# Performance work log

Measured on AMD Instinct MI355X. Metric: run time of the kernel, lower is better.

Reference implementation:

```python
import jax, jax.numpy as jnp
import numpy as np

P = 16        # patch size
SIM = 0.3     # similarity threshold (forward default arg `sim`)
STY_STD = 1000.0


def patchify(imgs):
    # (N,3,H,W) -> (N, h*w, p*p*3)
    N, C, H, W = imgs.shape
    h, w = H // P, W // P
    x = imgs.reshape(N, C, h, P, w, P)
    x = jnp.einsum('nchpwq->nhwpqc', x)
    return x.reshape(N, h * w, P * P * C)


def setup_inputs() -> dict:
    key = jax.random.key(0)
    k1, k2, k3, k4 = jax.random.split(key, 4)
    N, L, D = 2, 196, 768
    x = jax.random.normal(k1, (N, L + 1, D), dtype=jnp.float32)
    imgs = jax.random.normal(k2, (N, 3, 224, 224), dtype=jnp.float32)
    # torch trunc_normal_(std=1000, a=-2, b=2) == truncated normal on [-2,2]
    learnable_sty = (jax.random.truncated_normal(
        k3, -2.0 / STY_STD, 2.0 / STY_STD, (N, L, L, 1), dtype=jnp.float32) * STY_STD)
    noise = jax.random.normal(k4, (N, L, L, 1), dtype=jnp.float32)
    return {"x": x, "imgs": imgs, "learnable_sty": learnable_sty, "noise": noise}


def reference(x, imgs, learnable_sty, noise):
    imgs = patchify(imgs)                                   # (N, L, 768)
    cls_tokens, x = x[:, :1], x[:, 1:]
    N, L, D = x.shape

    # per-patch normalization (torch.var default is unbiased -> ddof=1)
    mean = imgs.mean(axis=-1, keepdims=True)
    var = jnp.var(imgs, axis=-1, keepdims=True, ddof=1)
    imgs_n = (imgs - mean) / jnp.sqrt(var + 1e-6)
    nrm = jnp.linalg.norm(imgs_n, axis=-1)                  # (N, L)
    Sim = jnp.einsum('aik,ajk->aij', imgs_n, imgs_n) / (nrm[:, :, None] * nrm[:, None, :])

    M0 = jnp.triu((Sim > SIM).astype(jnp.float32))          # (N, L, L), binary
    rows = jnp.arange(L)

    def body(i, M):
        # original loop breaks when sum == N*L; we freeze M once that holds
        done = M.sum() == N * L
        mask = (M[:, i, :] == 0).astype(M.dtype)            # (N, L)
        # rows <= i unchanged (M*M == M for binary), rows > i masked
        upd = jnp.where(rows[None, :, None] > i, M * mask[:, None, :], M)
        return jnp.where(done, M, upd)

    M = jax.lax.fori_loop(0, L - 1, body, M0)

    # decompose: phase (con) keeps grad, amplitude (sty) is detached
    fft = jnp.fft.fftn(x, axes=(-1,))
    con, sty = jnp.angle(fft), jnp.abs(fft)
    sty_d = jax.lax.stop_gradient(sty)

    avg_sum = (M[..., None] * sty_d[:, None, :, :]).sum(axis=2)   # (N, L, D)
    sty_mask = (avg_sum > 0).astype(jnp.float32)                   # (N, L, D)
    num = M.sum(axis=2)[..., None]                                 # (N, L, 1)
    avg = avg_sum / jnp.clip(num, 1e-7, None)                      # (N, L, D)
    std = jnp.sqrt(
        (M[..., None] * (sty_d[:, None, :, :] - avg[:, :, None, :]) ** 2).sum(axis=2)
        / jnp.clip(num, 1e-7, None))                               # (N, L, D)

    sty_para = sty_mask[:, None, :, :] * learnable_sty             # (N, L, L, D)
    sty_para = sty_para / jnp.clip(sty_para.sum(axis=2, keepdims=True), 1e-7, None)
    various = noise * std[:, None, :, :] + avg[:, None, :, :]      # (N, L, L, D)
    sum_sty = (sty_para * various).sum(axis=2)                     # (N, L, D)

    # compose: ifft(amp * e^{i phase}), torch .float() keeps the real part
    out = jnp.real(jnp.fft.ifftn(sum_sty * jnp.exp(1j * con), axes=(-1,))).astype(jnp.float32)
    return jnp.concatenate((cls_tokens, out), axis=1)
```

## Files before the change

kernel.cpp:

```cpp
#include <hip/hip_runtime.h>
#include <math.h>

typedef unsigned long long u64;

#define NBATCH 2
#define LTOK 196
#define DDIM 768
#define NROWS (NBATCH*LTOK)
#define NLD (NBATCH*LTOK*DDIM)

#define PI_F 3.14159265358979323846f
#define S3 0.86602540378443864676f

#define RTILE 14
#define JCH 4
#define JLEN 49
#define NCOMB (NBATCH*14*3*JCH)
#define GRIDB NROWS
#define NGRP 7
#define GSZ 56

#define SGRP 8
#define NSIMG 25
#define NSIMB (NBATCH*NSIMG)

__device__ __forceinline__ float aldf(const float* p) {
  unsigned u = __hip_atomic_load((const unsigned*)p, __ATOMIC_RELAXED,
                                 __HIP_MEMORY_SCOPE_AGENT);
  return __uint_as_float(u);
}
__device__ __forceinline__ void astf(float* p, float v) {
  __hip_atomic_store((unsigned*)p, __float_as_uint(v), __ATOMIC_RELAXED,
                     __HIP_MEMORY_SCOPE_AGENT);
}
__device__ __forceinline__ u64 ald64(const u64* p) {
  return __hip_atomic_load(p, __ATOMIC_RELAXED, __HIP_MEMORY_SCOPE_AGENT);
}
__device__ __forceinline__ void ast64(u64* p, u64 v) {
  __hip_atomic_store(p, v, __ATOMIC_RELAXED, __HIP_MEMORY_SCOPE_AGENT);
}

union ShMem {
  struct { float re[768]; float im[768]; float2 tw[128]; } fft;
  struct { double rs[4]; double rq[4]; float mu; float sc; } pat;
  struct { float simT[768][SGRP]; u64 gmask[SGRP][4]; int last; } sim2;
  struct { u64 Ml[NROWS*4]; int red[4]; int done; } gr;
  struct { u64 mrow[4]; } st;
  struct { float lsr[RTILE][JLEN], lnr[RTILE][JLEN]; } cmb;
};

__device__ __forceinline__ void gbar(unsigned* bar, int slot) {
  __syncthreads();
  if (threadIdx.x == 0) {
    unsigned* root = bar + (size_t)(slot * 8) * 32;
    unsigned* grp  = bar + (size_t)(slot * 8 + 1 + (blockIdx.x / GSZ)) * 32;
    if (__hip_atomic_fetch_add(grp, 1u, __ATOMIC_RELAXED,
                               __HIP_MEMORY_SCOPE_AGENT) == GSZ - 1u) {
      __hip_atomic_fetch_add(root, 1u, __ATOMIC_RELAXED,
                             __HIP_MEMORY_SCOPE_AGENT);
    }
    while (__hip_atomic_load(root, __ATOMIC_RELAXED,
                             __HIP_MEMORY_SCOPE_AGENT) < (unsigned)NGRP) {
      __builtin_amdgcn_s_sleep(8);
    }
  }
  __syncthreads();
}

__device__ __forceinline__ void fft_butterfly(float* re, float* im,
                                              const float2* T,
                                              int tau, int s, int half) {
  int sub = tau >> 7;
  int b = tau & 127;
  int j = b & (half - 1);
  int p0 = (sub << 8) + ((b >> (s - 1)) << s) + j;
  int p1 = p0 + half;
  float2 w = T[j << (8 - s)];
  float xr = re[p1], xi = im[p1];
  float tr = w.x * xr - w.y * xi;
  float ti = w.x * xi + w.y * xr;
  float ur = re[p0], ui = im[p0];
  re[p0] = ur + tr; im[p0] = ui + ti;
  re[p1] = ur - tr; im[p1] = ui - ti;
}

__device__ __forceinline__ void fft_stages(float* re, float* im,
                                           const float2* T, int t) {
#pragma unroll
  for (int s = 1; s <= 8; s++) {
    int half = 1 << (s - 1);
    fft_butterfly(re, im, T, t, s, half);
    if (t < 128) fft_butterfly(re, im, T, t + 256, s, half);
    __syncthreads();
  }
}

__device__ void greedy_block(u64* __restrict__ Mb, ShMem& sh) {
  int t = threadIdx.x;
  for (int w = t; w < NROWS * 4; w += 256) sh.gr.Ml[w] = ald64(&Mb[w]);
  __syncthreads();
  for (int i = 0; i < LTOK - 1; i++) {
    int s = 0;
    for (int w = t; w < NROWS * 4; w += 256) s += __popcll(sh.gr.Ml[w]);
#pragma unroll
    for (int o = 32; o > 0; o >>= 1) s += __shfl_down(s, o);
    if ((t & 63) == 0) sh.gr.red[t >> 6] = s;
    __syncthreads();
    if (t == 0)
      sh.gr.done = ((sh.gr.red[0] + sh.gr.red[1] + sh.gr.red[2] + sh.gr.red[3]) == NROWS) ? 1 : 0;
    __syncthreads();
    if (sh.gr.done) break;
    for (int w = t; w < NROWS * 4; w += 256) {
      int a = w / (LTOK * 4);
      int rem = w - a * (LTOK * 4);
      int r = rem >> 2, wi = rem & 3;
      if (r > i) sh.gr.Ml[w] &= ~sh.gr.Ml[(a * LTOK + i) * 4 + wi];
    }
    __syncthreads();
  }
  for (int w = t; w < NROWS * 4; w += 256) ast64(&Mb[w], sh.gr.Ml[w]);
}

__global__ __launch_bounds__(256, 2) void mega(
    const float* __restrict__ imgs, const float* __restrict__ x,
    const float* __restrict__ ls, const float* __restrict__ nz,
    float* __restrict__ out,
    float* __restrict__ uT, float* __restrict__ sty,
    float* __restrict__ phre, float* __restrict__ phim,
    float* __restrict__ sstd, float* __restrict__ smsk,
    float* __restrict__ numP, float* __restrict__ denP,
    u64* __restrict__ Mb, unsigned* __restrict__ bar) {
  __shared__ ShMem sh;
  const int t = threadIdx.x;
  const int blk = blockIdx.x;
  const int a = blk / LTOK, i = blk - (blk / LTOK) * LTOK;
  unsigned* ctr = bar + 32 * 32;

  {
    int hh = i / 14, ww = i - hh * 14;
    float loc[3];
    double s = 0.0, sq = 0.0;
#pragma unroll
    for (int e = 0; e < 3; e++) {
      int d = t + (e << 8);
      int p = d / 48, r = d - p * 48;
      int q2 = r / 3, c = r - q2 * 3;
      float val = imgs[((size_t)(a * 3 + c) * 224 + (hh * 16 + p)) * 224 + (ww * 16 + q2)];
      loc[e] = val;
      s += (double)val;
      sq += (double)val * (double)val;
    }
#pragma unroll
    for (int o = 32; o > 0; o >>= 1) { s += __shfl_down(s, o); sq += __shfl_down(sq, o); }
    if ((t & 63) == 0) { sh.pat.rs[t >> 6] = s; sh.pat.rq[t >> 6] = sq; }
    __syncthreads();
    if (t == 0) {
      double S = sh.pat.rs[0] + sh.pat.rs[1] + sh.pat.rs[2] + sh.pat.rs[3];
      double Q = sh.pat.rq[0] + sh.pat.rq[1] + sh.pat.rq[2] + sh.pat.rq[3];
      double mean = S / 768.0;
      double ss = Q - S * S / 768.0;
      if (ss < 1e-30) ss = 1e-30;
      sh.pat.mu = (float)mean;
      sh.pat.sc = (float)(1.0 / sqrt(ss));
    }
    __syncthreads();
    float mu = sh.pat.mu, sc = sh.pat.sc;
    int col = a * LTOK + i;
#pragma unroll
    for (int e = 0; e < 3; e++) {
      int d = t + (e << 8);
      astf(&uT[(size_t)d * NROWS + col], (loc[e] - mu) * sc);
    }
  }
  __syncthreads();

  {
    if (t < 128) {
      float sn, cs;
      __sincosf(-2.0f * PI_F * (float)t / 256.0f, &sn, &cs);
      sh.fft.tw[t] = make_float2(cs, sn);
    }
    size_t row = ((size_t)a * (LTOK + 1) + 1 + i) * DDIM;
#pragma unroll
    for (int e = 0; e < 3; e++) {
      int d = t + (e << 8);
      int m = d / 3, r = d - 3 * m;
      int p = (r << 8) + (__brev((unsigned)m) >> 24);
      sh.fft.re[p] = x[row + d];
      sh.fft.im[p] = 0.f;
    }
    __syncthreads();
    fft_stages(sh.fft.re, sh.fft.im, sh.fft.tw, t);
    float a0r = sh.fft.re[t],       a0i = sh.fft.im[t];
    float a1r = sh.fft.re[256 + t], a1i = sh.fft.im[256 + t];
    float a2r = sh.fft.re[512 + t], a2i = sh.fft.im[512 + t];
    float sn, cs;
    __sincosf(-2.0f * PI_F * (float)t / 768.0f, &sn, &cs);
    float2 w1 = make_float2(cs, sn);
    float2 w2 = make_float2(cs * cs - sn * sn, 2.f * cs * sn);
    float b1r = a1r * w1.x - a1i * w1.y, b1i = a1r * w1.y + a1i * w1.x;
    float b2r = a2r * w2.x - a2i * w2.y, b2i = a2r * w2.y + a2i * w2.x;
    float Xr[3], Xi[3];
    Xr[0] = a0r + b1r + b2r;
    Xi[0] = a0i + b1i + b2i;
    Xr[1] = a0r + (-0.5f * b1r + S3 * b1i) + (-0.5f * b2r - S3 * b2i);
    Xi[1] = a0i + (-0.5f * b1i - S3 * b1r) + (-0.5f * b2i + S3 * b2r);
    Xr[2] = a0r + (-0.5f * b1r - S3 * b1i) + (-0.5f * b2r + S3 * b2i);
    Xi[2] = a0i + (-0.5f * b1i + S3 * b1r) + (-0.5f * b2i - S3 * b2r);
    size_t ob = ((size_t)a * LTOK + i) * DDIM + t;
#pragma unroll
    for (int s2 = 0; s2 < 3; s2++) {
      float mag = sqrtf(Xr[s2] * Xr[s2] + Xi[s2] * Xi[s2]);
      size_t o = ob + (s2 << 8);
      astf(&sty[o], mag);
      if (mag > 0.f) { astf(&phre[o], Xr[s2] / mag); astf(&phim[o], Xi[s2] / mag); }
      else           { astf(&phre[o], 1.f);          astf(&phim[o], 0.f);          }
    }
  }
  gbar(bar, 0);

  if (blk < NSIMB) {
    int sa = blk / NSIMG, grp = blk - sa * NSIMG;
    int i0 = grp * SGRP;
    int nrow = (LTOK - i0 < SGRP) ? (LTOK - i0) : SGRP;
    int base = sa * LTOK + i0;
    for (int idx = t; idx < SGRP * 4; idx += 256) ((u64*)sh.sim2.gmask)[idx] = 0ull;
    for (int idx = t; idx < 768 * SGRP; idx += 256) {
      int d = idx >> 3, r = idx & 7;
      sh.sim2.simT[d][r] = (r < nrow) ? aldf(&uT[(size_t)d * NROWS + base + r]) : 0.f;
    }
    __syncthreads();
    int j = i0 + t;
    if (j < LTOK) {
      const float* colp = uT + sa * LTOK + j;
      float acc[SGRP];
#pragma unroll
      for (int k = 0; k < SGRP; k++) acc[k] = 0.f;
      for (int d0 = 0; d0 < 768; d0 += 16) {
        float cv[16];
#pragma unroll
        for (int q = 0; q < 16; q++) cv[q] = aldf(colp + (size_t)(d0 + q) * NROWS);
#pragma unroll
        for (int q = 0; q < 16; q++) {
          float4 A0 = *(const float4*)&sh.sim2.simT[d0 + q][0];
          float4 A1 = *(const float4*)&sh.sim2.simT[d0 + q][4];
          acc[0] += A0.x * cv[q]; acc[1] += A0.y * cv[q];
          acc[2] += A0.z * cv[q]; acc[3] += A0.w * cv[q];
          acc[4] += A1.x * cv[q]; acc[5] += A1.y * cv[q];
          acc[6] += A1.z * cv[q]; acc[7] += A1.w * cv[q];
        }
      }
#pragma unroll
      for (int k = 0; k < SGRP; k++) {
        int ii = i0 + k;
        if (k < nrow && j >= ii && acc[k] > 0.3f)
          atomicOr(&sh.sim2.gmask[k][j >> 6], 1ull << (j & 63));
      }
    }
    __syncthreads();
    if (t < nrow * 4)
      ast64(&Mb[((size_t)(base + (t >> 2))) * 4 + (t & 3)], sh.sim2.gmask[t >> 2][t & 3]);
    __syncthreads();
    if (t == 0)
      sh.sim2.last = (__hip_atomic_fetch_add(ctr, 1u, __ATOMIC_RELAXED,
                                             __HIP_MEMORY_SCOPE_AGENT) == NSIMB - 1u) ? 1 : 0;
    __syncthreads();
    int amlast = sh.sim2.last;
    __syncthreads();
    if (amlast) greedy_block(Mb, sh);
  }
  gbar(bar, 1);

  {
    float* savg = uT;
    if (t < 4) sh.st.mrow[t] = ald64(&Mb[((size_t)a * LTOK + i) * 4 + t]);
    __syncthreads();
    int num = __popcll(sh.st.mrow[0]) + __popcll(sh.st.mrow[1]) +
              __popcll(sh.st.mrow[2]) + __popcll(sh.st.mrow[3]);
    float fnum = fmaxf((float)num, 1e-7f);
    float acc0 = 0.f, acc1 = 0.f, acc2 = 0.f;
    for (int w = 0; w < 4; w++) {
      u64 m = sh.st.mrow[w];
      while (m) {
        int b = __ffsll(m) - 1; m &= (m - 1);
        int jj = (w << 6) + b;
        const float* sr = sty + ((size_t)a * LTOK + jj) * DDIM;
        acc0 += aldf(&sr[t]); acc1 += aldf(&sr[t + 256]); acc2 += aldf(&sr[t + 512]);
      }
    }
    float av0 = acc0 / fnum, av1 = acc1 / fnum, av2 = acc2 / fnum;
    float sq0 = 0.f, sq1 = 0.f, sq2 = 0.f;
    for (int w = 0; w < 4; w++) {
      u64 m = sh.st.mrow[w];
      while (m) {
        int b = __ffsll(m) - 1; m &= (m - 1);
        int jj = (w << 6) + b;
        const float* sr = sty + ((size_t)a * LTOK + jj) * DDIM;
        float e0 = aldf(&sr[t]) - av0, e1 = aldf(&sr[t + 256]) - av1, e2 = aldf(&sr[t + 512]) - av2;
        sq0 += e0 * e0; sq1 += e1 * e1; sq2 += e2 * e2;
      }
    }
    size_t o = ((size_t)a * LTOK + i) * DDIM + t;
    float mk0 = acc0 > 0.f ? 1.f : 0.f;
    float mk1 = acc1 > 0.f ? 1.f : 0.f;
    float mk2 = acc2 > 0.f ? 1.f : 0.f;
    astf(&smsk[o], mk0);           astf(&smsk[o + 256], mk1);           astf(&smsk[o + 512], mk2);
    astf(&savg[o], mk0 * av0);     astf(&savg[o + 256], mk1 * av1);     astf(&savg[o + 512], mk2 * av2);
    astf(&sstd[o], mk0 * sqrtf(sq0 / fnum));
    astf(&sstd[o + 256], mk1 * sqrtf(sq1 / fnum));
    astf(&sstd[o + 512], mk2 * sqrtf(sq2 / fnum));
  }
  gbar(bar, 2);

  if (blk < NCOMB) {
    const float* savg = uT;
    int ea = blk / 168;
    int rem = blk - ea * 168;
    int it = rem / 12;
    int r2 = rem - it * 12;
    int dc = r2 >> 2;
    int jc = r2 & 3;
    int i0 = it * RTILE;
    int j0 = jc * JLEN;
    int d = (dc << 8) + t;
    for (int idx = t; idx < RTILE * JLEN; idx += 256) {
      int ii = idx / JLEN, j = idx - ii * JLEN;
      size_t o = ((size_t)(ea * LTOK + i0 + ii)) * LTOK + j0 + j;
      float l = ls[o];
      sh.cmb.lsr[ii][j] = l;
      sh.cmb.lnr[ii][j] = l * nz[o];
    }
    __syncthreads();
    float nm[RTILE], dn[RTILE];
#pragma unroll
    for (int ii = 0; ii < RTILE; ii++) { nm[ii] = 0.f; dn[ii] = 0.f; }
#pragma unroll 7
    for (int j = 0; j < JLEN; j++) {
      size_t b = ((size_t)(ea * LTOK + j0 + j)) * DDIM + d;
      float sd = aldf(&sstd[b]), sv = aldf(&savg[b]), sm = aldf(&smsk[b]);
#pragma unroll
      for (int ii = 0; ii < RTILE; ii++) {
        nm[ii] += sh.cmb.lnr[ii][j] * sd;
        nm[ii] += sh.cmb.lsr[ii][j] * sv;
        dn[ii] += sh.cmb.lsr[ii][j] * sm;
      }
    }
#pragma unroll
    for (int ii = 0; ii < RTILE; ii++) {
      size_t o = ((size_t)jc * NROWS + (ea * LTOK + i0 + ii)) * DDIM + d;
      astf(&numP[o], nm[ii]);
      astf(&denP[o], dn[ii]);
    }
  }
  gbar(bar, 3);

  {
    if (blk < NBATCH) {
      size_t b = (size_t)blk * (LTOK + 1) * DDIM;
      out[b + t] = x[b + t];
      out[b + t + 256] = x[b + t + 256];
      out[b + t + 512] = x[b + t + 512];
    }
    if (t < 128) {
      float sn, cs;
      __sincosf(2.0f * PI_F * (float)t / 256.0f, &sn, &cs);
      sh.fft.tw[t] = make_float2(cs, sn);
    }
    size_t rowz = ((size_t)a * LTOK + i) * DDIM;
#pragma unroll
    for (int e = 0; e < 3; e++) {
      int d = t + (e << 8);
      float num = 0.f, den = 0.f;
#pragma unroll
      for (int jc = 0; jc < JCH; jc++) {
        size_t o = (size_t)jc * NROWS * DDIM + rowz + d;
        num += aldf(&numP[o]);
        den += aldf(&denP[o]);
      }
      float mg = num / fmaxf(den, 1e-7f);
      int m = d / 3, r = d - 3 * m;
      int p = (r << 8) + (__brev((unsigned)m) >> 24);
      sh.fft.re[p] = mg * aldf(&phre[rowz + d]);
      sh.fft.im[p] = mg * aldf(&phim[rowz + d]);
    }
    __syncthreads();
    fft_stages(sh.fft.re, sh.fft.im, sh.fft.tw, t);
    float a0r = sh.fft.re[t],       a0i = sh.fft.im[t];
    float a1r = sh.fft.re[256 + t], a1i = sh.fft.im[256 + t];
    float a2r = sh.fft.re[512 + t], a2i = sh.fft.im[512 + t];
    float sn, cs;
    __sincosf(2.0f * PI_F * (float)t / 768.0f, &sn, &cs);
    float2 w1 = make_float2(cs, sn);
    float2 w2 = make_float2(cs * cs - sn * sn, 2.f * cs * sn);
    float b1r = a1r * w1.x - a1i * w1.y, b1i = a1r * w1.y + a1i * w1.x;
    float b2r = a2r * w2.x - a2i * w2.y, b2i = a2r * w2.y + a2i * w2.x;
    float Xr[3];
    Xr[0] = a0r + b1r + b2r;
    Xr[1] = a0r + (-0.5f * b1r - S3 * b1i) + (-0.5f * b2r + S3 * b2i);
    Xr[2] = a0r + (-0.5f * b1r + S3 * b1i) + (-0.5f * b2r - S3 * b2i);
    size_t ob = ((size_t)a * (LTOK + 1) + 1 + i) * DDIM + t;
    const float inv = 1.0f / 768.0f;
    out[ob]       = Xr[0] * inv;
    out[ob + 256] = Xr[1] * inv;
    out[ob + 512] = Xr[2] * inv;
  }
}

extern "C" void kernel_launch(void* const* d_in, const int* in_sizes, int n_in,
                              void* d_out, int out_size, void* d_ws, size_t ws_size,
                              hipStream_t stream) {
  (void)in_sizes; (void)n_in; (void)out_size; (void)ws_size;
  const float* x    = (const float*)d_in[0];
  const float* imgs = (const float*)d_in[1];
  const float* ls   = (const float*)d_in[2];
  const float* nz   = (const float*)d_in[3];
  float* out = (float*)d_out;

  float* wf   = (float*)d_ws;
  float* uT   = wf;
  float* sty  = wf + (size_t)NLD;
  float* phre = wf + 2 * (size_t)NLD;
  float* phim = wf + 3 * (size_t)NLD;
  float* sstd = wf + 4 * (size_t)NLD;
  float* smsk = wf + 5 * (size_t)NLD;
  float* numP = wf + 6 * (size_t)NLD;
  float* denP = wf + 10 * (size_t)NLD;
  u64* Mb = (u64*)(wf + 14 * (size_t)NLD);
  unsigned* bar = (unsigned*)(Mb + (size_t)NROWS * 4);

  hipMemsetAsync((void*)bar, 0, 33 * 128, stream);

  mega<<<GRIDB, 256, 0, stream>>>(imgs, x, ls, nz, out,
                                  uT, sty, phre, phim, sstd, smsk,
                                  numP, denP, Mb, bar);
}
```

Before: 147.3 us.

## Store normalized patches row-major and recompute similarity with 4-row groups over all columns

The normalized patch matrix is now stored row-major instead of transposed. The similarity stage uses 98 blocks of 4 rows each instead of 50 blocks of 8 rows. Each thread computes dot products against a full row j for all 196 columns, not only j >= i0, so it reads a contiguous row instead of strided column entries. The intent is to spread the similarity work over more blocks and give each block fewer rows, but each thread's 768-float row read is uncoalesced across a warp, and work below the diagonal is no longer skipped.

```diff
diff --git a/kernel.cpp b/kernel.cpp
--- a/kernel.cpp
+++ b/kernel.cpp
@@ -20,8 +20,8 @@
 #define NGRP 7
 #define GSZ 56
 
-#define SGRP 8
-#define NSIMG 25
+#define IGRP 4
+#define NSIMG 49
 #define NSIMB (NBATCH*NSIMG)
 
 __device__ __forceinline__ float aldf(const float* p) {
@@ -43,7 +43,7 @@
 union ShMem {
   struct { float re[768]; float im[768]; float2 tw[128]; } fft;
   struct { double rs[4]; double rq[4]; float mu; float sc; } pat;
-  struct { float simT[768][SGRP]; u64 gmask[SGRP][4]; int last; } sim2;
+  struct { float simL[IGRP][DDIM]; u64 gmask[IGRP][4]; int last; } sim3;
   struct { u64 Ml[NROWS*4]; int red[4]; int done; } gr;
   struct { u64 mrow[4]; } st;
   struct { float lsr[RTILE][JLEN], lnr[RTILE][JLEN]; } cmb;
@@ -125,7 +125,7 @@
     const float* __restrict__ imgs, const float* __restrict__ x,
     const float* __restrict__ ls, const float* __restrict__ nz,
     float* __restrict__ out,
-    float* __restrict__ uT, float* __restrict__ sty,
+    float* __restrict__ u, float* __restrict__ sty,
     float* __restrict__ phre, float* __restrict__ phim,
     float* __restrict__ sstd, float* __restrict__ smsk,
     float* __restrict__ numP, float* __restrict__ denP,
@@ -165,11 +165,10 @@
     }
     __syncthreads();
     float mu = sh.pat.mu, sc = sh.pat.sc;
-    int col = a * LTOK + i;
 #pragma unroll
     for (int e = 0; e < 3; e++) {
       int d = t + (e << 8);
-      astf(&uT[(size_t)d * NROWS + col], (loc[e] - mu) * sc);
+      astf(&u[(size_t)blk * DDIM + d], (loc[e] - mu) * sc);
     }
   }
   __syncthreads();
@@ -221,58 +220,53 @@
 
   if (blk < NSIMB) {
     int sa = blk / NSIMG, grp = blk - sa * NSIMG;
-    int i0 = grp * SGRP;
-    int nrow = (LTOK - i0 < SGRP) ? (LTOK - i0) : SGRP;
+    int i0 = grp * IGRP;
     int base = sa * LTOK + i0;
-    for (int idx = t; idx < SGRP * 4; idx += 256) ((u64*)sh.sim2.gmask)[idx] = 0ull;
-    for (int idx = t; idx < 768 * SGRP; idx += 256) {
-      int d = idx >> 3, r = idx & 7;
-      sh.sim2.simT[d][r] = (r < nrow) ? aldf(&uT[(size_t)d * NROWS + base + r]) : 0.f;
-    }
-    __syncthreads();
-    int j = i0 + t;
+    if (t < IGRP * 4) sh.sim3.gmask[t >> 2][t & 3] = 0ull;
+    for (int idx = t; idx < IGRP * DDIM; idx += 256) {
+      int r = idx / DDIM, d = idx - r * DDIM;
+      sh.sim3.simL[r][d] = aldf(&u[(size_t)(base + r) * DDIM + d]);
+    }
+    __syncthreads();
+    int j = t;
     if (j < LTOK) {
-      const float* colp = uT + sa * LTOK + j;
-      float acc[SGRP];
-#pragma unroll
-      for (int k = 0; k < SGRP; k++) acc[k] = 0.f;
-      for (int d0 = 0; d0 < 768; d0 += 16) {
-        float cv[16];
-#pragma unroll
-        for (int q = 0; q < 16; q++) cv[q] = aldf(colp + (size_t)(d0 + q) * NROWS);
-#pragma unroll
-        for (int q = 0; q < 16; q++) {
-          float4 A0 = *(const float4*)&sh.sim2.simT[d0 + q][0];
-          float4 A1 = *(const float4*)&sh.sim2.simT[d0 + q][4];
-          acc[0] += A0.x * cv[q]; acc[1] += A0.y * cv[q];
-          acc[2] += A0.z * cv[q]; acc[3] += A0.w * cv[q];
-          acc[4] += A1.x * cv[q]; acc[5] += A1.y * cv[q];
-          acc[6] += A1.z * cv[q]; acc[7] += A1.w * cv[q];
+      const float* rowj = u + (size_t)(sa * LTOK + j) * DDIM;
+      float a0 = 0.f, a1 = 0.f, a2 = 0.f, a3 = 0.f;
+      for (int d0 = 0; d0 < DDIM; d0 += 32) {
+        float cv[32];
+#pragma unroll
+        for (int q = 0; q < 32; q++) cv[q] = aldf(rowj + d0 + q);
+#pragma unroll
+        for (int q = 0; q < 32; q++) {
+          float v = cv[q];
+          a0 += sh.sim3.simL[0][d0 + q] * v;
+          a1 += sh.sim3.simL[1][d0 + q] * v;
+          a2 += sh.sim3.simL[2][d0 + q] * v;
+          a3 += sh.sim3.simL[3][d0 + q] * v;
         }
       }
-#pragma unroll
-      for (int k = 0; k < SGRP; k++) {
-        int ii = i0 + k;
-        if (k < nrow && j >= ii && acc[k] > 0.3f)
-          atomicOr(&sh.sim2.gmask[k][j >> 6], 1ull << (j & 63));
-      }
-    }
-    __syncthreads();
-    if (t < nrow * 4)
-      ast64(&Mb[((size_t)(base + (t >> 2))) * 4 + (t & 3)], sh.sim2.gmask[t >> 2][t & 3]);
+      float accs[IGRP] = {a0, a1, a2, a3};
+#pragma unroll
+      for (int r = 0; r < IGRP; r++)
+        if (j >= i0 + r && accs[r] > 0.3f)
+          atomicOr(&sh.sim3.gmask[r][j >> 6], 1ull << (j & 63));
+    }
+    __syncthreads();
+    if (t < IGRP * 4)
+      ast64(&Mb[(size_t)(base + (t >> 2)) * 4 + (t & 3)], sh.sim3.gmask[t >> 2][t & 3]);
     __syncthreads();
     if (t == 0)
-      sh.sim2.last = (__hip_atomic_fetch_add(ctr, 1u, __ATOMIC_RELAXED,
+      sh.sim3.last = (__hip_atomic_fetch_add(ctr, 1u, __ATOMIC_RELAXED,
                                              __HIP_MEMORY_SCOPE_AGENT) == NSIMB - 1u) ? 1 : 0;
     __syncthreads();
-    int amlast = sh.sim2.last;
+    int amlast = sh.sim3.last;
     __syncthreads();
     if (amlast) greedy_block(Mb, sh);
   }
   gbar(bar, 1);
 
   {
-    float* savg = uT;
+    float* savg = u;
     if (t < 4) sh.st.mrow[t] = ald64(&Mb[((size_t)a * LTOK + i) * 4 + t]);
     __syncthreads();
     int num = __popcll(sh.st.mrow[0]) + __popcll(sh.st.mrow[1]) +
@@ -313,7 +307,7 @@
   gbar(bar, 2);
 
   if (blk < NCOMB) {
-    const float* savg = uT;
+    const float* savg = u;
     int ea = blk / 168;
     int rem = blk - ea * 168;
     int it = rem / 12;
@@ -417,7 +411,7 @@
   float* out = (float*)d_out;
 
   float* wf   = (float*)d_ws;
-  float* uT   = wf;
+  float* u    = wf;
   float* sty  = wf + (size_t)NLD;
   float* phre = wf + 2 * (size_t)NLD;
   float* phim = wf + 3 * (size_t)NLD;
@@ -431,6 +425,6 @@
   hipMemsetAsync((void*)bar, 0, 33 * 128, stream);
 
   mega<<<GRIDB, 256, 0, stream>>>(imgs, x, ls, nz, out,
-                                  uT, sty, phre, phim, sstd, smsk,
+                                  u, sty, phre, phim, sstd, smsk,
                                   numP, denP, Mb, bar);
 }
```

Result: slower. 204.3 us (+38.7%).
